# Kernel tuning notes

Measured on AMD Instinct MI355X. Metric: run time of the kernel, lower is better.

Reference implementation:

```python
import jax, jax.numpy as jnp
import numpy as np

N_NODES = 100000
N_EDGES = 1600000
D_IN, D_H, D_OUT = 256, 128, 128


def setup_inputs() -> dict:
    key = jax.random.key(0)
    ks = jax.random.split(key, 8)
    x = jax.random.normal(ks[0], (N_NODES, D_IN), dtype=jnp.float32)
    edge_index = jax.random.randint(ks[1], (2, N_EDGES), 0, N_NODES, dtype=jnp.int64)
    def glorot(k, fan_in, fan_out):
        s = jnp.sqrt(6.0 / (fan_in + fan_out))
        return jax.random.uniform(k, (fan_in, fan_out), jnp.float32, -s, s)
    W1 = glorot(ks[2], D_IN, D_H)
    b1 = jnp.zeros((D_H,), jnp.float32)
    W2 = glorot(ks[3], D_H, D_H)
    b2 = jnp.zeros((D_H,), jnp.float32)
    W3 = glorot(ks[4], D_H, D_OUT)
    b3 = jnp.zeros((D_OUT,), jnp.float32)
    return {"x": x, "edge_index": edge_index,
            "W1": W1, "b1": b1, "W2": W2, "b2": b2, "W3": W3, "b3": b3}


def _gcn_norm(edge_index, n_nodes):
    # PyG GCNConv: add self-loops, symmetric normalization D^-1/2 (A+I) D^-1/2
    loop = jnp.arange(n_nodes, dtype=edge_index.dtype)
    src = jnp.concatenate([edge_index[0], loop])  # source j
    dst = jnp.concatenate([edge_index[1], loop])  # target i
    deg = jax.ops.segment_sum(jnp.ones_like(dst, dtype=jnp.float32), dst,
                              num_segments=n_nodes)
    dinv = jnp.where(deg > 0, jax.lax.rsqrt(deg), 0.0)
    norm = dinv[src] * dinv[dst]  # [E+N]
    return src, dst, norm


def _gcn_conv(h, W, b, src, dst, norm, n_nodes):
    h = h @ W                                   # [N, d_out] transform first
    msg = h[src] * norm[:, None]                # gather + edge-weight
    out = jax.ops.segment_sum(msg, dst, num_segments=n_nodes)  # scatter-add
    return out + b


def reference(x, edge_index, W1, b1, W2, b2, W3, b3):
    n = x.shape[0]
    src, dst, norm = _gcn_norm(edge_index, n)
    h = jax.nn.relu(_gcn_conv(x, W1, b1, src, dst, norm, n))
    h = jax.nn.relu(_gcn_conv(h, W2, b2, src, dst, norm, n))
    return _gcn_conv(h, W3, b3, src, dst, norm, n)
```

## Files before the change

### kernel.cpp

```cpp
#include <hip/hip_runtime.h>
#include <hip/hip_fp16.h>
#include <math.h>


#define N_NODES 100000
#define N_EDGES 1600000

typedef _Float16 f16x8 __attribute__((ext_vector_type(8)));
typedef float    f32x4 __attribute__((ext_vector_type(4)));


__global__ __launch_bounds__(256) void k_zero_int(int* __restrict__ p, int n) {
    int i = blockIdx.x * 256 + threadIdx.x;
    if (i < n) p[i] = 0;
}

__global__ __launch_bounds__(256) void k_count(const int* __restrict__ dst, int* __restrict__ cnt, int E) {
    int e = blockIdx.x * 256 + threadIdx.x;
    if (e < E) atomicAdd(&cnt[dst[e]], 1);
}

__global__ __launch_bounds__(256) void k_scan_block(const int* __restrict__ cnt, int* __restrict__ excl,
                                                    int* __restrict__ bsum, int n) {
    __shared__ int s[256];
    int i = blockIdx.x * 256 + threadIdx.x;
    int v = (i < n) ? ((cnt[i] + 7) & ~7) : 0;
    s[threadIdx.x] = v;
    __syncthreads();
    #pragma unroll
    for (int off = 1; off < 256; off <<= 1) {
        int t = (threadIdx.x >= (unsigned)off) ? s[threadIdx.x - off] : 0;
        __syncthreads();
        s[threadIdx.x] += t;
        __syncthreads();
    }
    if (i < n) excl[i] = s[threadIdx.x] - v;
    if (threadIdx.x == 255) bsum[blockIdx.x] = s[255];
}

__global__ __launch_bounds__(512) void k_scan_partials(int* __restrict__ bsum, int nb) {
    __shared__ int s[512];
    int tid = threadIdx.x;
    int v = (tid < nb) ? bsum[tid] : 0;
    s[tid] = v;
    __syncthreads();
    #pragma unroll
    for (int off = 1; off < 512; off <<= 1) {
        int t = (tid >= (unsigned)off) ? s[tid - off] : 0;
        __syncthreads();
        s[tid] += t;
        __syncthreads();
    }
    if (tid < nb) bsum[tid] = s[tid] - v;
}

__global__ __launch_bounds__(256) void k_finalize(const int* __restrict__ excl, const int* __restrict__ bsum,
                                                  const int* __restrict__ cnt, int* __restrict__ rowptr,
                                                  int* __restrict__ fill, float* __restrict__ dinv, int n) {
    int i = blockIdx.x * 256 + threadIdx.x;
    if (i < n) {
        int rp = excl[i] + bsum[i >> 8];
        rowptr[i] = rp;
        fill[i]   = rp;
        dinv[i]   = rsqrtf((float)(cnt[i] + 1));
    }
}

__global__ __launch_bounds__(256) void k_init_csr(int* __restrict__ csr, int n, unsigned int* __restrict__ phz) {
    int i = blockIdx.x * 256 + threadIdx.x;
    if (i < n) csr[i] = N_NODES;
    if (blockIdx.x == 0 && threadIdx.x < 64) phz[threadIdx.x] = 0;
}

__global__ __launch_bounds__(256) void k_fill_edges(const int* __restrict__ src, const int* __restrict__ dst,
                                                    int* __restrict__ fill, int* __restrict__ csr,
                                                    int E, int lo, int hi) {
    int e = blockIdx.x * 256 + threadIdx.x;
    if (e < E) {
        int d = dst[e];
        if (d >= lo && d < hi) {
            int p = atomicAdd(&fill[d], 1);
            csr[p] = src[e];
        }
    }
}

__global__ __launch_bounds__(256) void k_wpack(const float* __restrict__ W, _Float16* __restrict__ Wpk, int K) {
    int j = blockIdx.x * 256 + threadIdx.x;
    if (j < K * 128) {
        int i  = j & 7;
        int l  = (j >> 3) & 63;
        int tc = (j >> 9) & 7;
        int c  = j >> 12;
        int col = tc * 16 + (l & 15);
        int k   = c * 32 + (l >> 4) * 8 + i;
        float w = W[(size_t)k * 128 + col];
        _Float16 h = (_Float16)w;
        Wpk[j] = h;
        Wpk[(size_t)K * 128 + j] = (_Float16)(w - (float)h);
    }
}


template <int K>
__global__ __launch_bounds__(256) void k_gemm_f32(const float* __restrict__ X,
                                                  const _Float16* __restrict__ Wpk,
                                                  const float* __restrict__ dinv,
                                                  _Float16* __restrict__ Y, int n) {
    constexpr int NS = K / 64;
    __shared__ float sX[64 * 64];
    const int t    = threadIdx.x;
    const int wave = t >> 6;
    const int lane = t & 63;
    const int lrow = lane & 15;
    const int kgrp = lane >> 4;
    const int row0 = blockIdx.x * 64;
    const int R    = wave * 16 + lrow;
    const _Float16* __restrict__ Wlo = Wpk + (size_t)K * 128;

    const int gsl = t & 15;
    const int rb  = t >> 4;
    const int r0 = rb, r1 = rb + 16, r2 = rb + 32, r3 = rb + 48;
    const int gc0 = ((gsl & 8) + ((gsl & 7) ^ (r0 & 7))) << 2;
    const int gc1 = ((gsl & 8) + ((gsl & 7) ^ (r1 & 7))) << 2;
    const int gc2 = ((gsl & 8) + ((gsl & 7) ^ (r2 & 7))) << 2;
    const int gc3 = ((gsl & 8) + ((gsl & 7) ^ (r3 & 7))) << 2;
    const bool ok0 = row0 + r0 < n, ok1 = row0 + r1 < n;
    const bool ok2 = row0 + r2 < n, ok3 = row0 + r3 < n;
    const float* __restrict__ xr0 = X + (size_t)(row0 + r0) * K;
    const float* __restrict__ xr1 = X + (size_t)(row0 + r1) * K;
    const float* __restrict__ xr2 = X + (size_t)(row0 + r2) * K;
    const float* __restrict__ xr3 = X + (size_t)(row0 + r3) * K;

    f32x4 acc[8];
    #pragma unroll
    for (int i = 0; i < 8; ++i) acc[i] = (f32x4){0.f, 0.f, 0.f, 0.f};

    const float4 z4 = make_float4(0.f, 0.f, 0.f, 0.f);
    float4 rv0 = ok0 ? *(const float4*)&xr0[gc0] : z4;
    float4 rv1 = ok1 ? *(const float4*)&xr1[gc1] : z4;
    float4 rv2 = ok2 ? *(const float4*)&xr2[gc2] : z4;
    float4 rv3 = ok3 ? *(const float4*)&xr3[gc3] : z4;
    *(float4*)&sX[(r0 * 16 + gsl) * 4] = rv0;
    *(float4*)&sX[(r1 * 16 + gsl) * 4] = rv1;
    *(float4*)&sX[(r2 * 16 + gsl) * 4] = rv2;
    *(float4*)&sX[(r3 * 16 + gsl) * 4] = rv3;
    __syncthreads();

    #pragma unroll
    for (int s = 0; s < NS; ++s) {
        if (s + 1 < NS) {
            const int o = (s + 1) * 64;
            rv0 = ok0 ? *(const float4*)&xr0[o + gc0] : z4;
            rv1 = ok1 ? *(const float4*)&xr1[o + gc1] : z4;
            rv2 = ok2 ? *(const float4*)&xr2[o + gc2] : z4;
            rv3 = ok3 ? *(const float4*)&xr3[o + gc3] : z4;
        }
        #pragma unroll
        for (int cc = 0; cc < 2; ++cc) {
            const int c = s * 2 + cc;
            float4 x0 = *(const float4*)&sX[(R * 16 + cc * 8 + ((kgrp * 2)     ^ (R & 7))) * 4];
            float4 x1 = *(const float4*)&sX[(R * 16 + cc * 8 + ((kgrp * 2 + 1) ^ (R & 7))) * 4];
            float xs[8] = {x0.x, x0.y, x0.z, x0.w, x1.x, x1.y, x1.z, x1.w};
            f16x8 ah, al;
            #pragma unroll
            for (int i = 0; i < 8; ++i) {
                _Float16 h = (_Float16)xs[i];
                ah[i] = h;
                al[i] = (_Float16)(xs[i] - (float)h);
            }
            const size_t wb = ((size_t)(c * 8) * 64 + lane) * 8;
            #pragma unroll
            for (int tc = 0; tc < 8; ++tc) {
                f16x8 bh = *(const f16x8*)(Wpk + wb + (size_t)tc * 512);
                f16x8 bl = *(const f16x8*)(Wlo + wb + (size_t)tc * 512);
                acc[tc] = __builtin_amdgcn_mfma_f32_16x16x32_f16(ah, bh, acc[tc], 0, 0, 0);
                acc[tc] = __builtin_amdgcn_mfma_f32_16x16x32_f16(al, bh, acc[tc], 0, 0, 0);
                acc[tc] = __builtin_amdgcn_mfma_f32_16x16x32_f16(ah, bl, acc[tc], 0, 0, 0);
            }
        }
        if (s + 1 < NS) {
            __syncthreads();
            *(float4*)&sX[(r0 * 16 + gsl) * 4] = rv0;
            *(float4*)&sX[(r1 * 16 + gsl) * 4] = rv1;
            *(float4*)&sX[(r2 * 16 + gsl) * 4] = rv2;
            *(float4*)&sX[(r3 * 16 + gsl) * 4] = rv3;
            __syncthreads();
        }
    }

    #pragma unroll
    for (int r = 0; r < 4; ++r) {
        int grow = row0 + wave * 16 + kgrp * 4 + r;
        if (grow < n) {
            float dv = dinv[grow];
            _Float16* yr = Y + (size_t)grow * 128 + lrow;
            #pragma unroll
            for (int tc = 0; tc < 8; ++tc) yr[tc * 16] = (_Float16)(dv * acc[tc][r]);
        }
    }
}


template <int K>
__global__ __launch_bounds__(256) void k_gemm_f16(const _Float16* __restrict__ X,
                                                  const _Float16* __restrict__ Wpk,
                                                  const float* __restrict__ dinv,
                                                  _Float16* __restrict__ Y, int n) {
    constexpr int NC = K / 32;
    __shared__ unsigned int sX[64 * 20];
    const int t    = threadIdx.x;
    const int wave = t >> 6;
    const int lane = t & 63;
    const int lrow = lane & 15;
    const int kgrp = lane >> 4;
    const int row0 = blockIdx.x * 64;
    const int R    = wave * 16 + lrow;
    const _Float16* __restrict__ Wlo = Wpk + (size_t)K * 128;

    const int sr = t >> 2, sg = t & 3;
    const bool sok = row0 + sr < n;
    const unsigned int* __restrict__ xrow = (const unsigned int*)(X + (size_t)(row0 + sr) * K);

    f32x4 acc[8];
    #pragma unroll
    for (int i = 0; i < 8; ++i) acc[i] = (f32x4){0.f, 0.f, 0.f, 0.f};

    const uint4 zu = make_uint4(0, 0, 0, 0);
    uint4 rv = sok ? *(const uint4*)&xrow[sg * 4] : zu;
    *(uint4*)&sX[sr * 20 + sg * 4] = rv;
    __syncthreads();

    #pragma unroll
    for (int c = 0; c < NC; ++c) {
        if (c + 1 < NC) rv = sok ? *(const uint4*)&xrow[(c + 1) * 16 + sg * 4] : zu;
        f16x8 a = *(const f16x8*)&sX[R * 20 + kgrp * 4];
        const size_t wb = ((size_t)(c * 8) * 64 + lane) * 8;
        #pragma unroll
        for (int tc = 0; tc < 8; ++tc) {
            f16x8 bh = *(const f16x8*)(Wpk + wb + (size_t)tc * 512);
            f16x8 bl = *(const f16x8*)(Wlo + wb + (size_t)tc * 512);
            acc[tc] = __builtin_amdgcn_mfma_f32_16x16x32_f16(a, bh, acc[tc], 0, 0, 0);
            acc[tc] = __builtin_amdgcn_mfma_f32_16x16x32_f16(a, bl, acc[tc], 0, 0, 0);
        }
        if (c + 1 < NC) {
            __syncthreads();
            *(uint4*)&sX[sr * 20 + sg * 4] = rv;
            __syncthreads();
        }
    }

    #pragma unroll
    for (int r = 0; r < 4; ++r) {
        int grow = row0 + wave * 16 + kgrp * 4 + r;
        if (grow < n) {
            float dv = dinv[grow];
            _Float16* yr = Y + (size_t)grow * 128 + lrow;
            #pragma unroll
            for (int tc = 0; tc < 8; ++tc) yr[tc * 16] = (_Float16)(dv * acc[tc][r]);
        }
    }
}


__device__ __forceinline__ void acc8(float a[8], uint4 u) {
    float2 p;
    p = __half22float2(*(__half2*)&u.x); a[0] += p.x; a[1] += p.y;
    p = __half22float2(*(__half2*)&u.y); a[2] += p.x; a[3] += p.y;
    p = __half22float2(*(__half2*)&u.z); a[4] += p.x; a[5] += p.y;
    p = __half22float2(*(__half2*)&u.w); a[6] += p.x; a[7] += p.y;
}

template <bool RELU, bool OUTF16>
__global__ __launch_bounds__(256) void k_agg(const __half* __restrict__ H, const int* __restrict__ rowptr,
                                             const int* __restrict__ cnt, const int* __restrict__ csr,
                                             const float* __restrict__ dinv, const float* __restrict__ bias,
                                             void* __restrict__ out, int n) {
    const int lane  = threadIdx.x & 63;
    const int q     = lane >> 4;
    const int fl    = lane & 15;
    const int wave0 = (int)((blockIdx.x * 256 + threadIdx.x) >> 6);
    const int nwave = (int)((gridDim.x * 256) >> 6);
    const uint4* __restrict__ Hu = (const uint4*)H;
    const float4 b0 = *(const float4*)&bias[fl * 8];
    const float4 b1 = *(const float4*)&bias[fl * 8 + 4];

    const int nquad = n >> 2;
    for (int g = wave0; g < nquad; g += nwave) {
        const int node = g * 4 + q;
        float a[8];
        {
            uint4 u = Hu[(size_t)node * 16 + fl];
            float2 p;
            p = __half22float2(*(__half2*)&u.x); a[0] = p.x; a[1] = p.y;
            p = __half22float2(*(__half2*)&u.y); a[2] = p.x; a[3] = p.y;
            p = __half22float2(*(__half2*)&u.z); a[4] = p.x; a[5] = p.y;
            p = __half22float2(*(__half2*)&u.w); a[6] = p.x; a[7] = p.y;
        }

        const int c0 = rowptr[node];
        const int cn = cnt[node];
        for (int e8 = 0; e8 < cn; e8 += 8) {
            const int4* qp = (const int4*)(csr + c0 + e8);
            int4 qa = qp[0], qb = qp[1];
            uint4 u0 = Hu[(size_t)qa.x * 16 + fl];
            uint4 u1 = Hu[(size_t)qa.y * 16 + fl];
            uint4 u2 = Hu[(size_t)qa.z * 16 + fl];
            uint4 u3 = Hu[(size_t)qa.w * 16 + fl];
            uint4 u4 = Hu[(size_t)qb.x * 16 + fl];
            uint4 u5 = Hu[(size_t)qb.y * 16 + fl];
            uint4 u6 = Hu[(size_t)qb.z * 16 + fl];
            uint4 u7 = Hu[(size_t)qb.w * 16 + fl];
            acc8(a, u0); acc8(a, u1); acc8(a, u2); acc8(a, u3);
            acc8(a, u4); acc8(a, u5); acc8(a, u6); acc8(a, u7);
        }

        const float dv = dinv[node];
        float o[8];
        o[0] = fmaf(dv, a[0], b0.x); o[1] = fmaf(dv, a[1], b0.y);
        o[2] = fmaf(dv, a[2], b0.z); o[3] = fmaf(dv, a[3], b0.w);
        o[4] = fmaf(dv, a[4], b1.x); o[5] = fmaf(dv, a[5], b1.y);
        o[6] = fmaf(dv, a[6], b1.z); o[7] = fmaf(dv, a[7], b1.w);
        if (RELU) {
            #pragma unroll
            for (int i = 0; i < 8; ++i) o[i] = fmaxf(o[i], 0.f);
        }
        if (OUTF16) {
            f16x8 hv;
            #pragma unroll
            for (int i = 0; i < 8; ++i) hv[i] = (_Float16)o[i];
            *(f16x8*)((_Float16*)out + (size_t)node * 128 + fl * 8) = hv;
        } else {
            float* op = (float*)out + (size_t)node * 128 + fl * 8;
            *(float4*)&op[0] = make_float4(o[0], o[1], o[2], o[3]);
            *(float4*)&op[4] = make_float4(o[4], o[5], o[6], o[7]);
        }
    }
}


extern "C" void kernel_launch(void* const* d_in, const int* in_sizes, int n_in,
                              void* d_out, int out_size, void* d_ws, size_t ws_size,
                              hipStream_t stream) {
    const float* x  = (const float*)d_in[0];
    const int*   ei = (const int*)d_in[1];
    const float* W1 = (const float*)d_in[2];
    const float* b1 = (const float*)d_in[3];
    const float* W2 = (const float*)d_in[4];
    const float* b2 = (const float*)d_in[5];
    const float* W3 = (const float*)d_in[6];
    const float* b3 = (const float*)d_in[7];
    float* out = (float*)d_out;

    const int N = N_NODES, E = N_EDGES;
    const int EP = E + 7 * N + 64;
    const int* src = ei;
    const int* dst = ei + E;

    char* w = (char*)d_ws;
    auto alloc = [&](size_t bytes) -> void* {
        void* p = (void*)w;
        w += (bytes + 255) & ~(size_t)255;
        return p;
    };
    int*      cnt    = (int*)alloc((size_t)N * 4);
    int*      excl   = (int*)alloc((size_t)N * 4);
    int*      bsum   = (int*)alloc(4096);
    int*      rowptr = (int*)alloc((size_t)N * 4);
    int*      fill   = (int*)alloc((size_t)N * 4);
    float*    dinv   = (float*)alloc((size_t)N * 4);
    int*      csr    = (int*)alloc((size_t)EP * 4);
    _Float16* Ph     = (_Float16*)alloc((size_t)(N + 8) * 128 * 2);
    _Float16* Qh     = (_Float16*)alloc((size_t)N * 128 * 2);
    _Float16* Wpk    = (_Float16*)alloc((size_t)2 * 256 * 128 * 2);

    const int nbN = (N + 255) / 256;
    const int nbE = (E + 255) / 256;
    const int nbP = (EP + 255) / 256;

    k_zero_int<<<nbN, 256, 0, stream>>>(cnt, N);
    k_count<<<nbE, 256, 0, stream>>>(dst, cnt, E);
    k_scan_block<<<nbN, 256, 0, stream>>>(cnt, excl, bsum, N);
    k_scan_partials<<<1, 512, 0, stream>>>(bsum, nbN);
    k_finalize<<<nbN, 256, 0, stream>>>(excl, bsum, cnt, rowptr, fill, dinv, N);
    k_init_csr<<<nbP, 256, 0, stream>>>(csr, EP, (unsigned int*)(Ph + (size_t)N * 128));
    for (int r = 0; r < 4; ++r) {
        int lo = r * (N / 4);
        int hi = (r == 3) ? N : (r + 1) * (N / 4);
        k_fill_edges<<<nbE, 256, 0, stream>>>(src, dst, fill, csr, E, lo, hi);
    }

    const int gemm_grid = (N + 63) / 64;
    const int agg_grid  = 2048;

    k_wpack<<<(256 * 128 + 255) / 256, 256, 0, stream>>>(W1, Wpk, 256);
    k_gemm_f32<256><<<gemm_grid, 256, 0, stream>>>(x, Wpk, dinv, Ph, N);
    k_agg<true, true><<<agg_grid, 256, 0, stream>>>((const __half*)Ph, rowptr, cnt, csr, dinv, b1, Qh, N);
    k_wpack<<<(128 * 128 + 255) / 256, 256, 0, stream>>>(W2, Wpk, 128);
    k_gemm_f16<128><<<gemm_grid, 256, 0, stream>>>(Qh, Wpk, dinv, Ph, N);
    k_agg<true, true><<<agg_grid, 256, 0, stream>>>((const __half*)Ph, rowptr, cnt, csr, dinv, b2, Qh, N);
    k_wpack<<<(128 * 128 + 255) / 256, 256, 0, stream>>>(W3, Wpk, 128);
    k_gemm_f16<128><<<gemm_grid, 256, 0, stream>>>(Qh, Wpk, dinv, Ph, N);
    k_agg<false, false><<<agg_grid, 256, 0, stream>>>((const __half*)Ph, rowptr, cnt, csr, dinv, b3, out, N);
}
```

Measured before the change: 459.1 us.

## Fuse degree counting into first GEMM and move source normalization into aggregation

The edge-degree counting kernel is folded into the first GEMM launch as extra blocks. This lets the first GEMM run before the degree scan, since it no longer needs dinv. The per-source dinv scaling moves from the GEMM epilogues into the aggregation, which now gathers dinv[src] per edge and uses FMA. That adds a scattered 4-byte load per edge in each of the three aggregations, and it pads dinv with a zero entry at index N for the padding-edge sentinel. It also removes a launch and lets the atomic counting overlap with GEMM work.

```diff
diff --git a/kernel.cpp b/kernel.cpp
--- a/kernel.cpp
+++ b/kernel.cpp
@@ -13,11 +13,6 @@
 __global__ __launch_bounds__(256) void k_zero_int(int* __restrict__ p, int n) {
     int i = blockIdx.x * 256 + threadIdx.x;
     if (i < n) p[i] = 0;
-}
-
-__global__ __launch_bounds__(256) void k_count(const int* __restrict__ dst, int* __restrict__ cnt, int E) {
-    int e = blockIdx.x * 256 + threadIdx.x;
-    if (e < E) atomicAdd(&cnt[dst[e]], 1);
 }
 
 __global__ __launch_bounds__(256) void k_scan_block(const int* __restrict__ cnt, int* __restrict__ excl,
@@ -66,10 +61,12 @@
     }
 }
 
-__global__ __launch_bounds__(256) void k_init_csr(int* __restrict__ csr, int n, unsigned int* __restrict__ phz) {
+__global__ __launch_bounds__(256) void k_init_csr(int* __restrict__ csr, int n, unsigned int* __restrict__ phz,
+                                                  float* __restrict__ dinvN) {
     int i = blockIdx.x * 256 + threadIdx.x;
     if (i < n) csr[i] = N_NODES;
     if (blockIdx.x == 0 && threadIdx.x < 64) phz[threadIdx.x] = 0;
+    if (blockIdx.x == 0 && threadIdx.x == 64) dinvN[0] = 0.f;
 }
 
 __global__ __launch_bounds__(256) void k_fill_edges(const int* __restrict__ src, const int* __restrict__ dst,
@@ -103,12 +100,18 @@
 
 
 template <int K>
-__global__ __launch_bounds__(256) void k_gemm_f32(const float* __restrict__ X,
-                                                  const _Float16* __restrict__ Wpk,
-                                                  const float* __restrict__ dinv,
-                                                  _Float16* __restrict__ Y, int n) {
+__global__ __launch_bounds__(256) void k_gemm1_count(const float* __restrict__ X,
+                                                     const _Float16* __restrict__ Wpk,
+                                                     _Float16* __restrict__ Y, int n,
+                                                     const int* __restrict__ dst, int* __restrict__ cnt,
+                                                     int E, int gemm_blocks) {
     constexpr int NS = K / 64;
     __shared__ float sX[64 * 64];
+    if ((int)blockIdx.x >= gemm_blocks) {
+        int e = (blockIdx.x - gemm_blocks) * 256 + threadIdx.x;
+        if (e < E) atomicAdd(&cnt[dst[e]], 1);
+        return;
+    }
     const int t    = threadIdx.x;
     const int wave = t >> 6;
     const int lane = t & 63;
@@ -193,10 +196,9 @@
     for (int r = 0; r < 4; ++r) {
         int grow = row0 + wave * 16 + kgrp * 4 + r;
         if (grow < n) {
-            float dv = dinv[grow];
             _Float16* yr = Y + (size_t)grow * 128 + lrow;
             #pragma unroll
-            for (int tc = 0; tc < 8; ++tc) yr[tc * 16] = (_Float16)(dv * acc[tc][r]);
+            for (int tc = 0; tc < 8; ++tc) yr[tc * 16] = (_Float16)acc[tc][r];
         }
     }
 }
@@ -205,7 +207,6 @@
 template <int K>
 __global__ __launch_bounds__(256) void k_gemm_f16(const _Float16* __restrict__ X,
                                                   const _Float16* __restrict__ Wpk,
-                                                  const float* __restrict__ dinv,
                                                   _Float16* __restrict__ Y, int n) {
     constexpr int NC = K / 32;
     __shared__ unsigned int sX[64 * 20];
@@ -254,21 +255,20 @@
     for (int r = 0; r < 4; ++r) {
         int grow = row0 + wave * 16 + kgrp * 4 + r;
         if (grow < n) {
-            float dv = dinv[grow];
             _Float16* yr = Y + (size_t)grow * 128 + lrow;
             #pragma unroll
-            for (int tc = 0; tc < 8; ++tc) yr[tc * 16] = (_Float16)(dv * acc[tc][r]);
-        }
-    }
-}
-
-
-__device__ __forceinline__ void acc8(float a[8], uint4 u) {
+            for (int tc = 0; tc < 8; ++tc) yr[tc * 16] = (_Float16)acc[tc][r];
+        }
+    }
+}
+
+
+__device__ __forceinline__ void facc8(float a[8], uint4 u, float w) {
     float2 p;
-    p = __half22float2(*(__half2*)&u.x); a[0] += p.x; a[1] += p.y;
-    p = __half22float2(*(__half2*)&u.y); a[2] += p.x; a[3] += p.y;
-    p = __half22float2(*(__half2*)&u.z); a[4] += p.x; a[5] += p.y;
-    p = __half22float2(*(__half2*)&u.w); a[6] += p.x; a[7] += p.y;
+    p = __half22float2(*(__half2*)&u.x); a[0] = fmaf(w, p.x, a[0]); a[1] = fmaf(w, p.y, a[1]);
+    p = __half22float2(*(__half2*)&u.y); a[2] = fmaf(w, p.x, a[2]); a[3] = fmaf(w, p.y, a[3]);
+    p = __half22float2(*(__half2*)&u.z); a[4] = fmaf(w, p.x, a[4]); a[5] = fmaf(w, p.y, a[5]);
+    p = __half22float2(*(__half2*)&u.w); a[6] = fmaf(w, p.x, a[6]); a[7] = fmaf(w, p.y, a[7]);
 }
 
 template <bool RELU, bool OUTF16>
@@ -288,14 +288,15 @@
     const int nquad = n >> 2;
     for (int g = wave0; g < nquad; g += nwave) {
         const int node = g * 4 + q;
+        const float dv = dinv[node];
         float a[8];
         {
             uint4 u = Hu[(size_t)node * 16 + fl];
             float2 p;
-            p = __half22float2(*(__half2*)&u.x); a[0] = p.x; a[1] = p.y;
-            p = __half22float2(*(__half2*)&u.y); a[2] = p.x; a[3] = p.y;
-            p = __half22float2(*(__half2*)&u.z); a[4] = p.x; a[5] = p.y;
-            p = __half22float2(*(__half2*)&u.w); a[6] = p.x; a[7] = p.y;
+            p = __half22float2(*(__half2*)&u.x); a[0] = dv * p.x; a[1] = dv * p.y;
+            p = __half22float2(*(__half2*)&u.y); a[2] = dv * p.x; a[3] = dv * p.y;
+            p = __half22float2(*(__half2*)&u.z); a[4] = dv * p.x; a[5] = dv * p.y;
+            p = __half22float2(*(__half2*)&u.w); a[6] = dv * p.x; a[7] = dv * p.y;
         }
 
         const int c0 = rowptr[node];
@@ -311,11 +312,12 @@
             uint4 u5 = Hu[(size_t)qb.y * 16 + fl];
             uint4 u6 = Hu[(size_t)qb.z * 16 + fl];
             uint4 u7 = Hu[(size_t)qb.w * 16 + fl];
-            acc8(a, u0); acc8(a, u1); acc8(a, u2); acc8(a, u3);
-            acc8(a, u4); acc8(a, u5); acc8(a, u6); acc8(a, u7);
-        }
-
-        const float dv = dinv[node];
+            float d0 = dinv[qa.x], d1 = dinv[qa.y], d2 = dinv[qa.z], d3 = dinv[qa.w];
+            float d4 = dinv[qb.x], d5 = dinv[qb.y], d6 = dinv[qb.z], d7 = dinv[qb.w];
+            facc8(a, u0, d0); facc8(a, u1, d1); facc8(a, u2, d2); facc8(a, u3, d3);
+            facc8(a, u4, d4); facc8(a, u5, d5); facc8(a, u6, d6); facc8(a, u7, d7);
+        }
+
         float o[8];
         o[0] = fmaf(dv, a[0], b0.x); o[1] = fmaf(dv, a[1], b0.y);
         o[2] = fmaf(dv, a[2], b0.z); o[3] = fmaf(dv, a[3], b0.w);
@@ -368,7 +370,7 @@
     int*      bsum   = (int*)alloc(4096);
     int*      rowptr = (int*)alloc((size_t)N * 4);
     int*      fill   = (int*)alloc((size_t)N * 4);
-    float*    dinv   = (float*)alloc((size_t)N * 4);
+    float*    dinv   = (float*)alloc((size_t)(N + 8) * 4);
     int*      csr    = (int*)alloc((size_t)EP * 4);
     _Float16* Ph     = (_Float16*)alloc((size_t)(N + 8) * 128 * 2);
     _Float16* Qh     = (_Float16*)alloc((size_t)N * 128 * 2);
@@ -377,29 +379,28 @@
     const int nbN = (N + 255) / 256;
     const int nbE = (E + 255) / 256;
     const int nbP = (EP + 255) / 256;
+    const int gemm_grid = (N + 63) / 64;
+    const int agg_grid  = 2048;
 
     k_zero_int<<<nbN, 256, 0, stream>>>(cnt, N);
-    k_count<<<nbE, 256, 0, stream>>>(dst, cnt, E);
+    k_wpack<<<(256 * 128 + 255) / 256, 256, 0, stream>>>(W1, Wpk, 256);
+    k_gemm1_count<256><<<gemm_grid + nbE, 256, 0, stream>>>(x, Wpk, Ph, N, dst, cnt, E, gemm_grid);
+
     k_scan_block<<<nbN, 256, 0, stream>>>(cnt, excl, bsum, N);
     k_scan_partials<<<1, 512, 0, stream>>>(bsum, nbN);
     k_finalize<<<nbN, 256, 0, stream>>>(excl, bsum, cnt, rowptr, fill, dinv, N);
-    k_init_csr<<<nbP, 256, 0, stream>>>(csr, EP, (unsigned int*)(Ph + (size_t)N * 128));
+    k_init_csr<<<nbP, 256, 0, stream>>>(csr, EP, (unsigned int*)(Ph + (size_t)N * 128), dinv + N);
     for (int r = 0; r < 4; ++r) {
         int lo = r * (N / 4);
         int hi = (r == 3) ? N : (r + 1) * (N / 4);
         k_fill_edges<<<nbE, 256, 0, stream>>>(src, dst, fill, csr, E, lo, hi);
     }
 
-    const int gemm_grid = (N + 63) / 64;
-    const int agg_grid  = 2048;
-
-    k_wpack<<<(256 * 128 + 255) / 256, 256, 0, stream>>>(W1, Wpk, 256);
-    k_gemm_f32<256><<<gemm_grid, 256, 0, stream>>>(x, Wpk, dinv, Ph, N);
     k_agg<true, true><<<agg_grid, 256, 0, stream>>>((const __half*)Ph, rowptr, cnt, csr, dinv, b1, Qh, N);
     k_wpack<<<(128 * 128 + 255) / 256, 256, 0, stream>>>(W2, Wpk, 128);
-    k_gemm_f16<128><<<gemm_grid, 256, 0, stream>>>(Qh, Wpk, dinv, Ph, N);
+    k_gemm_f16<128><<<gemm_grid, 256, 0, stream>>>(Qh, Wpk, Ph, N);
     k_agg<true, true><<<agg_grid, 256, 0, stream>>>((const __half*)Ph, rowptr, cnt, csr, dinv, b2, Qh, N);
     k_wpack<<<(128 * 128 + 255) / 256, 256, 0, stream>>>(W3, Wpk, 128);
-    k_gemm_f16<128><<<gemm_grid, 256, 0, stream>>>(Qh, Wpk, dinv, Ph, N);
+    k_gemm_f16<128><<<gemm_grid, 256, 0, stream>>>(Qh, Wpk, Ph, N);
     k_agg<false, false><<<agg_grid, 256, 0, stream>>>((const __half*)Ph, rowptr, cnt, csr, dinv, b3, out, N);
 }
```

Result: faster. 442.4 us (-3.6%).
